# Kernel optimization log

Hardware: AMD Instinct MI355X
Metric: run time of the kernel (lower is better)

The kernel has to match this reference:

```python
import jax, jax.numpy as jnp
import numpy as np

T, H, E, K, I = 4096, 1024, 8, 2, 2048
EPS = 1e-5


def setup_inputs() -> dict:
    key = jax.random.key(0)
    ks = jax.random.split(key, 5)
    xavier = jax.nn.initializers.variance_scaling(1.0, 'fan_avg', 'uniform', dtype=jnp.float32)
    return {
        'x': jax.random.normal(ks[0], (T, H), dtype=jnp.float32),
        'scale': jnp.ones((H,), dtype=jnp.float32),
        'gate_kernel': xavier(ks[1], (H, E), jnp.float32),
        'gate_bias': jnp.zeros((E,), dtype=jnp.float32),
        'mlp1_weight': xavier(ks[2], (E, 2 * I, H), jnp.float32),
        'mlp1_bias': jnp.zeros((E, 2 * I), dtype=jnp.float32),
        'mlp2_weight': xavier(ks[3], (E, H, I), jnp.float32),
        'mlp2_bias': jnp.zeros((E, H), dtype=jnp.float32),
    }


def reference(x, scale, gate_kernel, gate_bias, mlp1_weight, mlp1_bias, mlp2_weight, mlp2_bias):
    # RMSNorm in fp32
    t = x.astype(jnp.float32)
    rms = jnp.sqrt(jnp.mean(t * t, axis=-1, keepdims=True) + EPS)
    normed = ((t / rms) * scale).astype(x.dtype)  # [T, H]

    # Gating: top-k experts + softmax over selected logits
    gate_logits = normed @ gate_kernel + gate_bias  # [T, E]
    expert_logits, expert_indices = jax.lax.top_k(gate_logits, K)  # [T, K]
    expert_weights = jax.nn.softmax(expert_logits, axis=-1)  # [T, K]

    # Dense all-expert SwiGLU MLP (faithful to vmap-over-experts original)
    # mlp1_weight: [E, 2I, H] -> mlp1: [E, T, 2I]
    mlp1 = jnp.einsum('td,efd->etf', normed, mlp1_weight) + mlp1_bias[:, None, :]
    gate_part = jnp.minimum(mlp1[..., :I], 7.0)
    linear_part = jnp.clip(mlp1[..., I:], -7.0, 7.0)
    swish_gate = gate_part * jax.nn.sigmoid(1.702 * gate_part)
    activated = swish_gate * (linear_part + 1.0)  # [E, T, I]
    # mlp2_weight: [E, H, I] -> expert_outputs: [T, E, H]
    expert_outputs = (jnp.einsum('eti,ehi->eth', activated, mlp2_weight)
                      + mlp2_bias[:, None, :]).transpose(1, 0, 2)

    # Scatter top-k weights to dense [T, E] and combine
    one_hot = jax.nn.one_hot(expert_indices, E, dtype=expert_outputs.dtype)  # [T, K, E]
    dense_gate_weights = jnp.sum(one_hot * expert_weights[..., None], axis=1)  # [T, E]
    fused = jnp.einsum('teh,te->th', expert_outputs, dense_gate_weights)
    return x + fused
```

## Files before the change

kernel.cpp:

```cpp
#include <hip/hip_runtime.h>
#include <hip/hip_bf16.h>
#include <math.h>

#define T_ 4096
#define H_ 1024
#define E_ 8
#define I_ 2048
#define EPS_ 1e-5f
#define LDST 72

using bf16x8 = __attribute__((ext_vector_type(8))) short;
using f32x4  = __attribute__((ext_vector_type(4))) float;

static __device__ __forceinline__ unsigned short f2bf(float f) {
    union { float f; unsigned int u; } v; v.f = f;
    unsigned int u = v.u;
    u += 0x7fffu + ((u >> 16) & 1u);
    return (unsigned short)(u >> 16);
}

__global__ __launch_bounds__(256) void k_convert(
    const float* __restrict__ src, unsigned short* __restrict__ dst)
{
    size_t i = (size_t)blockIdx.x * 256 + threadIdx.x;
    const float4* s = (const float4*)src + i * 2;
    float4 a = s[0], b = s[1];
    ushort4 lo, hi;
    lo.x = f2bf(a.x); lo.y = f2bf(a.y); lo.z = f2bf(a.z); lo.w = f2bf(a.w);
    hi.x = f2bf(b.x); hi.y = f2bf(b.y); hi.z = f2bf(b.z); hi.w = f2bf(b.w);
    ((ushort4*)dst)[i * 2]     = lo;
    ((ushort4*)dst)[i * 2 + 1] = hi;
}

__global__ __launch_bounds__(256) void k_norm_gate(
    const float* __restrict__ x, const float* __restrict__ scale,
    const float* __restrict__ gk, const float* __restrict__ gb,
    unsigned short* __restrict__ normed_bf,
    int* __restrict__ counts, int* __restrict__ tok_list, float* __restrict__ w_list)
{
    int tid = threadIdx.x;
    int wave = tid >> 6, lane = tid & 63;
    int t = blockIdx.x * 4 + wave;
    const float* xr = x + (size_t)t * H_;
    int h0 = lane * 16;

    float4 xv[4], sv[4];
    #pragma unroll
    for (int c = 0; c < 4; c++) {
        xv[c] = *(const float4*)(xr + h0 + c * 4);
        sv[c] = *(const float4*)(scale + h0 + c * 4);
    }
    float ss = 0.f;
    #pragma unroll
    for (int c = 0; c < 4; c++)
        ss += xv[c].x*xv[c].x + xv[c].y*xv[c].y + xv[c].z*xv[c].z + xv[c].w*xv[c].w;
    #pragma unroll
    for (int off = 32; off; off >>= 1) ss += __shfl_xor(ss, off);
    float inv = 1.0f / sqrtf(ss / (float)H_ + EPS_);

    float nv[16];
    #pragma unroll
    for (int c = 0; c < 4; c++) {
        nv[c*4+0] = xv[c].x * inv * sv[c].x;
        nv[c*4+1] = xv[c].y * inv * sv[c].y;
        nv[c*4+2] = xv[c].z * inv * sv[c].z;
        nv[c*4+3] = xv[c].w * inv * sv[c].w;
    }
    #pragma unroll
    for (int c = 0; c < 4; c++) {
        ushort4 nb;
        nb.x = f2bf(nv[c*4+0]); nb.y = f2bf(nv[c*4+1]);
        nb.z = f2bf(nv[c*4+2]); nb.w = f2bf(nv[c*4+3]);
        *(ushort4*)(normed_bf + (size_t)t * H_ + h0 + c * 4) = nb;
    }

    float p[E_];
    #pragma unroll
    for (int e = 0; e < E_; e++) p[e] = 0.f;
    #pragma unroll
    for (int j = 0; j < 16; j++) {
        const float4* g4 = (const float4*)(gk + (size_t)(h0 + j) * E_);
        float4 a = g4[0], b = g4[1];
        float n = nv[j];
        p[0] += n*a.x; p[1] += n*a.y; p[2] += n*a.z; p[3] += n*a.w;
        p[4] += n*b.x; p[5] += n*b.y; p[6] += n*b.z; p[7] += n*b.w;
    }
    #pragma unroll
    for (int e = 0; e < E_; e++) {
        #pragma unroll
        for (int off = 32; off; off >>= 1) p[e] += __shfl_xor(p[e], off);
    }
    if (lane == 0) {
        int b0 = -1, b1 = -1; float l0 = -1e30f, l1 = -1e30f;
        #pragma unroll
        for (int e = 0; e < E_; e++) {
            float lg = p[e] + gb[e];
            if (lg > l0) { l1 = l0; b1 = b0; l0 = lg; b0 = e; }
            else if (lg > l1) { l1 = lg; b1 = e; }
        }
        float e1 = expf(l1 - l0);
        float w0 = 1.f / (1.f + e1);
        float w1 = e1 / (1.f + e1);
        int p0 = atomicAdd(&counts[b0], 1);
        tok_list[b0 * T_ + p0] = t * 2 + 0; w_list[b0 * T_ + p0] = w0;
        int p1 = atomicAdd(&counts[b1], 1);
        tok_list[b1 * T_ + p1] = t * 2 + 1; w_list[b1 * T_ + p1] = w1;
    }
}

__global__ __launch_bounds__(256) void k_init_out(
    const float* __restrict__ x, float* __restrict__ out)
{
    size_t i = (size_t)blockIdx.x * 256 + threadIdx.x;
    ((float4*)out)[i] = ((const float4*)x)[i];
}

template<bool PRE>
__global__ __launch_bounds__(256) void k_mlp1(
    const float* __restrict__ w1f, const unsigned short* __restrict__ w1b,
    const float* __restrict__ b1,
    const unsigned short* __restrict__ normed_bf,
    const int* __restrict__ counts, const int* __restrict__ tok_list,
    unsigned short* __restrict__ act)
{
    int e = blockIdx.z;
    int Ne = counts[e];
    int mt0 = blockIdx.y * 64;
    if (mt0 >= Ne) return;
    int it0 = blockIdx.x * 64;
    int tid = threadIdx.x;
    int lane = tid & 63, w = tid >> 6;
    int quad = lane >> 4, m16 = lane & 15;
    int wr = w >> 1, wc = w & 1;

    __shared__ unsigned short lA[64 * LDST];
    __shared__ unsigned short lBg[64 * LDST];
    __shared__ unsigned short lBl[64 * LDST];
    __shared__ int ls_tk[64];

    if (tid < 64) {
        int slot = mt0 + tid;
        ls_tk[tid] = (slot < Ne) ? tok_list[e * T_ + slot] : -1;
    }
    __syncthreads();

    f32x4 accg[2][2], accl[2][2];
    #pragma unroll
    for (int mi = 0; mi < 2; mi++)
        #pragma unroll
        for (int ni = 0; ni < 2; ni++) {
            accg[mi][ni] = (f32x4){0.f, 0.f, 0.f, 0.f};
            accl[mi][ni] = (f32x4){0.f, 0.f, 0.f, 0.f};
        }

    const size_t w1base = (size_t)e * 2 * I_ * H_;
    int rA = tid >> 3, sgA = tid & 7;
    int nB = tid >> 2, sgB = tid & 3;

    if (PRE) {
        int tk0 = ls_tk[rA], tk1 = ls_tk[rA + 32];
        const unsigned short* sA0 = normed_bf + (size_t)((tk0 < 0) ? 0 : (tk0 >> 1)) * H_ + sgA * 8;
        const unsigned short* sA1 = normed_bf + (size_t)((tk1 < 0) ? 0 : (tk1 >> 1)) * H_ + sgA * 8;
        const unsigned short* sG = w1b + w1base + (size_t)(it0 + nB) * H_ + sgB * 16;
        const unsigned short* sL = sG + (size_t)I_ * H_;

        uint4 ra0, ra1, rg0, rg1, rl0, rl1;
        ra0 = (tk0 >= 0) ? *(const uint4*)(sA0) : make_uint4(0,0,0,0);
        ra1 = (tk1 >= 0) ? *(const uint4*)(sA1) : make_uint4(0,0,0,0);
        rg0 = ((const uint4*)sG)[0]; rg1 = ((const uint4*)sG)[1];
        rl0 = ((const uint4*)sL)[0]; rl1 = ((const uint4*)sL)[1];

        for (int kk = 0; kk < H_; kk += 64) {
            __syncthreads();
            *(uint4*)(&lA[rA * LDST + sgA * 8])          = ra0;
            *(uint4*)(&lA[(rA + 32) * LDST + sgA * 8])   = ra1;
            *(uint4*)(&lBg[nB * LDST + sgB * 16])        = rg0;
            *(uint4*)(&lBg[nB * LDST + sgB * 16 + 8])    = rg1;
            *(uint4*)(&lBl[nB * LDST + sgB * 16])        = rl0;
            *(uint4*)(&lBl[nB * LDST + sgB * 16 + 8])    = rl1;
            __syncthreads();
            if (kk + 64 < H_) {
                int k2 = kk + 64;
                ra0 = (tk0 >= 0) ? *(const uint4*)(sA0 + k2) : make_uint4(0,0,0,0);
                ra1 = (tk1 >= 0) ? *(const uint4*)(sA1 + k2) : make_uint4(0,0,0,0);
                rg0 = ((const uint4*)(sG + k2))[0]; rg1 = ((const uint4*)(sG + k2))[1];
                rl0 = ((const uint4*)(sL + k2))[0]; rl1 = ((const uint4*)(sL + k2))[1];
            }
            #pragma unroll
            for (int ks = 0; ks < 64; ks += 32) {
                bf16x8 af[2], bg[2], bl[2];
                #pragma unroll
                for (int mi = 0; mi < 2; mi++)
                    af[mi] = *(const bf16x8*)(&lA[(wr * 32 + mi * 16 + m16) * LDST + ks + quad * 8]);
                #pragma unroll
                for (int ni = 0; ni < 2; ni++) {
                    bg[ni] = *(const bf16x8*)(&lBg[(wc * 32 + ni * 16 + m16) * LDST + ks + quad * 8]);
                    bl[ni] = *(const bf16x8*)(&lBl[(wc * 32 + ni * 16 + m16) * LDST + ks + quad * 8]);
                }
                #pragma unroll
                for (int mi = 0; mi < 2; mi++)
                    #pragma unroll
                    for (int ni = 0; ni < 2; ni++) {
                        accg[mi][ni] = __builtin_amdgcn_mfma_f32_16x16x32_bf16(
                            af[mi], bg[ni], accg[mi][ni], 0, 0, 0);
                        accl[mi][ni] = __builtin_amdgcn_mfma_f32_16x16x32_bf16(
                            af[mi], bl[ni], accl[mi][ni], 0, 0, 0);
                    }
            }
        }
    } else {
        for (int kk = 0; kk < H_; kk += 64) {
            #pragma unroll
            for (int rr = 0; rr < 64; rr += 32) {
                int r = rA + rr;
                int tk = ls_tk[r];
                uint4 v = make_uint4(0u, 0u, 0u, 0u);
                if (tk >= 0)
                    v = *(const uint4*)(normed_bf + (size_t)(tk >> 1) * H_ + kk + sgA * 8);
                *(uint4*)(&lA[r * LDST + sgA * 8]) = v;
            }
            {
                const float* srcg = w1f + w1base + (size_t)(it0 + nB) * H_ + kk + sgB * 16;
                const float* srcl = srcg + (size_t)I_ * H_;
                unsigned short tg[16], tl[16];
                #pragma unroll
                for (int q = 0; q < 4; q++) {
                    float4 fg = ((const float4*)srcg)[q];
                    float4 fl = ((const float4*)srcl)[q];
                    tg[q*4+0] = f2bf(fg.x); tg[q*4+1] = f2bf(fg.y);
                    tg[q*4+2] = f2bf(fg.z); tg[q*4+3] = f2bf(fg.w);
                    tl[q*4+0] = f2bf(fl.x); tl[q*4+1] = f2bf(fl.y);
                    tl[q*4+2] = f2bf(fl.z); tl[q*4+3] = f2bf(fl.w);
                }
                *(uint4*)(&lBg[nB * LDST + sgB * 16])     = *(uint4*)(&tg[0]);
                *(uint4*)(&lBg[nB * LDST + sgB * 16 + 8]) = *(uint4*)(&tg[8]);
                *(uint4*)(&lBl[nB * LDST + sgB * 16])     = *(uint4*)(&tl[0]);
                *(uint4*)(&lBl[nB * LDST + sgB * 16 + 8]) = *(uint4*)(&tl[8]);
            }
            __syncthreads();
            #pragma unroll
            for (int ks = 0; ks < 64; ks += 32) {
                bf16x8 af[2], bg[2], bl[2];
                #pragma unroll
                for (int mi = 0; mi < 2; mi++)
                    af[mi] = *(const bf16x8*)(&lA[(wr * 32 + mi * 16 + m16) * LDST + ks + quad * 8]);
                #pragma unroll
                for (int ni = 0; ni < 2; ni++) {
                    bg[ni] = *(const bf16x8*)(&lBg[(wc * 32 + ni * 16 + m16) * LDST + ks + quad * 8]);
                    bl[ni] = *(const bf16x8*)(&lBl[(wc * 32 + ni * 16 + m16) * LDST + ks + quad * 8]);
                }
                #pragma unroll
                for (int mi = 0; mi < 2; mi++)
                    #pragma unroll
                    for (int ni = 0; ni < 2; ni++) {
                        accg[mi][ni] = __builtin_amdgcn_mfma_f32_16x16x32_bf16(
                            af[mi], bg[ni], accg[mi][ni], 0, 0, 0);
                        accl[mi][ni] = __builtin_amdgcn_mfma_f32_16x16x32_bf16(
                            af[mi], bl[ni], accl[mi][ni], 0, 0, 0);
                    }
            }
            __syncthreads();
        }
    }

    const float* b1g = b1 + (size_t)e * 2 * I_;
    const float* b1l = b1g + I_;
    #pragma unroll
    for (int mi = 0; mi < 2; mi++) {
        #pragma unroll
        for (int reg = 0; reg < 4; reg++) {
            int row = wr * 32 + mi * 16 + quad * 4 + reg;
            int tk = ls_tk[row];
            if (tk < 0) continue;
            #pragma unroll
            for (int ni = 0; ni < 2; ni++) {
                int i = it0 + wc * 32 + ni * 16 + m16;
                float g = accg[mi][ni][reg] + b1g[i];
                float l = accl[mi][ni][reg] + b1l[i];
                g = fminf(g, 7.f);
                l = fminf(fmaxf(l, -7.f), 7.f);
                float sw = g / (1.f + expf(-1.702f * g));
                act[(size_t)tk * I_ + i] = f2bf(sw * (l + 1.f));
            }
        }
    }
}

template<bool PRE>
__global__ __launch_bounds__(256) void k_mlp2(
    const float* __restrict__ w2f, const unsigned short* __restrict__ w2b,
    const float* __restrict__ b2,
    const unsigned short* __restrict__ act,
    const int* __restrict__ counts, const int* __restrict__ tok_list,
    const float* __restrict__ w_list,
    float* __restrict__ out)
{
    int e = blockIdx.z;
    int Ne = counts[e];
    int mt0 = blockIdx.y * 64;
    if (mt0 >= Ne) return;
    int ht0 = blockIdx.x * 128;
    int tid = threadIdx.x;
    int lane = tid & 63, w = tid >> 6;
    int quad = lane >> 4, m16 = lane & 15;
    int wr = w >> 1, wc = w & 1;

    __shared__ unsigned short lA[64 * LDST];
    __shared__ unsigned short lB[128 * LDST];
    __shared__ int ls_tk[64];
    __shared__ float ls_w[64];

    if (tid < 64) {
        int slot = mt0 + tid;
        ls_tk[tid] = (slot < Ne) ? tok_list[e * T_ + slot] : -1;
        ls_w[tid]  = (slot < Ne) ? w_list[e * T_ + slot] : 0.f;
    }
    __syncthreads();

    f32x4 acc[2][4];
    #pragma unroll
    for (int mi = 0; mi < 2; mi++)
        #pragma unroll
        for (int ni = 0; ni < 4; ni++)
            acc[mi][ni] = (f32x4){0.f, 0.f, 0.f, 0.f};

    const size_t w2base = (size_t)e * H_ * I_;
    int rA = tid >> 3, sgA = tid & 7;
    int nB = tid >> 2, sgB = tid & 3;

    if (PRE) {
        int tk0 = ls_tk[rA], tk1 = ls_tk[rA + 32];
        const unsigned short* sA0 = act + (size_t)((tk0 < 0) ? 0 : tk0) * I_ + sgA * 8;
        const unsigned short* sA1 = act + (size_t)((tk1 < 0) ? 0 : tk1) * I_ + sgA * 8;
        const unsigned short* sB0 = w2b + w2base + (size_t)(ht0 + nB) * I_ + sgB * 16;
        const unsigned short* sB1 = sB0 + (size_t)64 * I_;

        uint4 ra0, ra1, rb00, rb01, rb10, rb11;
        ra0 = (tk0 >= 0) ? *(const uint4*)(sA0) : make_uint4(0,0,0,0);
        ra1 = (tk1 >= 0) ? *(const uint4*)(sA1) : make_uint4(0,0,0,0);
        rb00 = ((const uint4*)sB0)[0]; rb01 = ((const uint4*)sB0)[1];
        rb10 = ((const uint4*)sB1)[0]; rb11 = ((const uint4*)sB1)[1];

        for (int kk = 0; kk < I_; kk += 64) {
            __syncthreads();
            *(uint4*)(&lA[rA * LDST + sgA * 8])            = ra0;
            *(uint4*)(&lA[(rA + 32) * LDST + sgA * 8])     = ra1;
            *(uint4*)(&lB[nB * LDST + sgB * 16])           = rb00;
            *(uint4*)(&lB[nB * LDST + sgB * 16 + 8])       = rb01;
            *(uint4*)(&lB[(nB + 64) * LDST + sgB * 16])    = rb10;
            *(uint4*)(&lB[(nB + 64) * LDST + sgB * 16 + 8])= rb11;
            __syncthreads();
            if (kk + 64 < I_) {
                int k2 = kk + 64;
                ra0 = (tk0 >= 0) ? *(const uint4*)(sA0 + k2) : make_uint4(0,0,0,0);
                ra1 = (tk1 >= 0) ? *(const uint4*)(sA1 + k2) : make_uint4(0,0,0,0);
                rb00 = ((const uint4*)(sB0 + k2))[0]; rb01 = ((const uint4*)(sB0 + k2))[1];
                rb10 = ((const uint4*)(sB1 + k2))[0]; rb11 = ((const uint4*)(sB1 + k2))[1];
            }
            #pragma unroll
            for (int ks = 0; ks < 64; ks += 32) {
                bf16x8 af[2], bf[4];
                #pragma unroll
                for (int mi = 0; mi < 2; mi++)
                    af[mi] = *(const bf16x8*)(&lA[(wr * 32 + mi * 16 + m16) * LDST + ks + quad * 8]);
                #pragma unroll
                for (int ni = 0; ni < 4; ni++)
                    bf[ni] = *(const bf16x8*)(&lB[(wc * 64 + ni * 16 + m16) * LDST + ks + quad * 8]);
                #pragma unroll
                for (int mi = 0; mi < 2; mi++)
                    #pragma unroll
                    for (int ni = 0; ni < 4; ni++)
                        acc[mi][ni] = __builtin_amdgcn_mfma_f32_16x16x32_bf16(
                            af[mi], bf[ni], acc[mi][ni], 0, 0, 0);
            }
        }
    } else {
        for (int kk = 0; kk < I_; kk += 64) {
            #pragma unroll
            for (int rr = 0; rr < 64; rr += 32) {
                int r = rA + rr;
                int tk = ls_tk[r];
                uint4 v = make_uint4(0u, 0u, 0u, 0u);
                if (tk >= 0)
                    v = *(const uint4*)(act + (size_t)tk * I_ + kk + sgA * 8);
                *(uint4*)(&lA[r * LDST + sgA * 8]) = v;
            }
            #pragma unroll
            for (int rr = 0; rr < 128; rr += 64) {
                int r = nB + rr;
                const float* src = w2f + w2base + (size_t)(ht0 + r) * I_ + kk + sgB * 16;
                unsigned short tb[16];
                #pragma unroll
                for (int q = 0; q < 4; q++) {
                    float4 f4 = ((const float4*)src)[q];
                    tb[q*4+0] = f2bf(f4.x); tb[q*4+1] = f2bf(f4.y);
                    tb[q*4+2] = f2bf(f4.z); tb[q*4+3] = f2bf(f4.w);
                }
                *(uint4*)(&lB[r * LDST + sgB * 16])     = *(uint4*)(&tb[0]);
                *(uint4*)(&lB[r * LDST + sgB * 16 + 8]) = *(uint4*)(&tb[8]);
            }
            __syncthreads();
            #pragma unroll
            for (int ks = 0; ks < 64; ks += 32) {
                bf16x8 af[2], bf[4];
                #pragma unroll
                for (int mi = 0; mi < 2; mi++)
                    af[mi] = *(const bf16x8*)(&lA[(wr * 32 + mi * 16 + m16) * LDST + ks + quad * 8]);
                #pragma unroll
                for (int ni = 0; ni < 4; ni++)
                    bf[ni] = *(const bf16x8*)(&lB[(wc * 64 + ni * 16 + m16) * LDST + ks + quad * 8]);
                #pragma unroll
                for (int mi = 0; mi < 2; mi++)
                    #pragma unroll
                    for (int ni = 0; ni < 4; ni++)
                        acc[mi][ni] = __builtin_amdgcn_mfma_f32_16x16x32_bf16(
                            af[mi], bf[ni], acc[mi][ni], 0, 0, 0);
            }
            __syncthreads();
        }
    }

    const float* b2e = b2 + (size_t)e * H_;
    #pragma unroll
    for (int mi = 0; mi < 2; mi++) {
        #pragma unroll
        for (int reg = 0; reg < 4; reg++) {
            int row = wr * 32 + mi * 16 + quad * 4 + reg;
            int tk = ls_tk[row];
            if (tk < 0) continue;
            int t = tk >> 1;
            float wgt = ls_w[row];
            #pragma unroll
            for (int ni = 0; ni < 4; ni++) {
                int h = ht0 + wc * 64 + ni * 16 + m16;
                float v = acc[mi][ni][reg] + b2e[h];
                atomicAdd(&out[(size_t)t * H_ + h], wgt * v);
            }
        }
    }
}

extern "C" void kernel_launch(void* const* d_in, const int* in_sizes, int n_in,
                              void* d_out, int out_size, void* d_ws, size_t ws_size,
                              hipStream_t stream) {
    const float* x     = (const float*)d_in[0];
    const float* scale = (const float*)d_in[1];
    const float* gk    = (const float*)d_in[2];
    const float* gb    = (const float*)d_in[3];
    const float* w1    = (const float*)d_in[4];
    const float* b1    = (const float*)d_in[5];
    const float* w2    = (const float*)d_in[6];
    const float* b2    = (const float*)d_in[7];
    float* out = (float*)d_out;

    char* ws = (char*)d_ws;
    const size_t MB = 1024 * 1024;
    bool pre = ws_size >= (size_t)138 * MB;

    unsigned short* normed_bf = (unsigned short*)ws;
    unsigned short* act       = (unsigned short*)(ws + 8 * MB);
    unsigned short* w1b = nullptr;
    unsigned short* w2b = nullptr;
    char* ctl;
    if (pre) {
        w1b = (unsigned short*)(ws + 40 * MB);
        w2b = (unsigned short*)(ws + 104 * MB);
        ctl = ws + 136 * MB;
    } else {
        ctl = ws + 40 * MB;
    }
    int*   counts   = (int*)ctl;
    int*   tok_list = (int*)(ctl + 256);
    float* w_list   = (float*)(ctl + 256 + (size_t)E_ * T_ * 4);

    hipMemsetAsync(counts, 0, E_ * sizeof(int), stream);

    k_norm_gate<<<dim3(T_ / 4), dim3(256), 0, stream>>>(x, scale, gk, gb,
                                                        normed_bf, counts, tok_list, w_list);
    if (pre) {
        k_convert<<<dim3((E_ * 2 * I_ * H_) / (256 * 8)), dim3(256), 0, stream>>>(w1, w1b);
        k_convert<<<dim3((E_ * H_ * I_) / (256 * 8)), dim3(256), 0, stream>>>(w2, w2b);
    }
    k_init_out<<<dim3(T_ * H_ / (256 * 4)), dim3(256), 0, stream>>>(x, out);

    if (pre) {
        k_mlp1<true><<<dim3(I_ / 64, T_ / 64, E_), dim3(256), 0, stream>>>(
            nullptr, w1b, b1, normed_bf, counts, tok_list, act);
        k_mlp2<true><<<dim3(H_ / 128, T_ / 64, E_), dim3(256), 0, stream>>>(
            nullptr, w2b, b2, act, counts, tok_list, w_list, out);
    } else {
        k_mlp1<false><<<dim3(I_ / 64, T_ / 64, E_), dim3(256), 0, stream>>>(
            w1, nullptr, b1, normed_bf, counts, tok_list, act);
        k_mlp2<false><<<dim3(H_ / 128, T_ / 64, E_), dim3(256), 0, stream>>>(
            w2, nullptr, b2, act, counts, tok_list, w_list, out);
    }
}
```

Baseline: 599.8 us.

## Replace atomic scatter with per-slot output buffer and combine; swizzle LDS tiles

The second expert GEMM now writes each token-slot result with its bias to a dense buffer instead of atomically adding weighted results into the output. A new combine kernel then forms x + w0*y0 + w1*y1 per token, and the init-output copy is removed. Shared-memory tiles switch from padded rows to an XOR-swizzled 64-element layout to avoid bank conflicts with less LDS. The fp32-weight fallback path is dropped, so the kernel now assumes a large workspace, and the new buffer reuses memory of the converted first-layer weights.

```diff
diff --git a/kernel.cpp b/kernel.cpp
--- a/kernel.cpp
+++ b/kernel.cpp
@@ -7,7 +7,6 @@
 #define E_ 8
 #define I_ 2048
 #define EPS_ 1e-5f
-#define LDST 72
 
 using bf16x8 = __attribute__((ext_vector_type(8))) short;
 using f32x4  = __attribute__((ext_vector_type(4))) float;
@@ -36,7 +35,7 @@
     const float* __restrict__ x, const float* __restrict__ scale,
     const float* __restrict__ gk, const float* __restrict__ gb,
     unsigned short* __restrict__ normed_bf,
-    int* __restrict__ counts, int* __restrict__ tok_list, float* __restrict__ w_list)
+    int* __restrict__ counts, int* __restrict__ tok_list, float* __restrict__ wtok)
 {
     int tid = threadIdx.x;
     int wave = tid >> 6, lane = tid & 63;
@@ -101,23 +100,17 @@
         float e1 = expf(l1 - l0);
         float w0 = 1.f / (1.f + e1);
         float w1 = e1 / (1.f + e1);
+        wtok[t * 2 + 0] = w0;
+        wtok[t * 2 + 1] = w1;
         int p0 = atomicAdd(&counts[b0], 1);
-        tok_list[b0 * T_ + p0] = t * 2 + 0; w_list[b0 * T_ + p0] = w0;
+        tok_list[b0 * T_ + p0] = t * 2 + 0;
         int p1 = atomicAdd(&counts[b1], 1);
-        tok_list[b1 * T_ + p1] = t * 2 + 1; w_list[b1 * T_ + p1] = w1;
-    }
-}
-
-__global__ __launch_bounds__(256) void k_init_out(
-    const float* __restrict__ x, float* __restrict__ out)
-{
-    size_t i = (size_t)blockIdx.x * 256 + threadIdx.x;
-    ((float4*)out)[i] = ((const float4*)x)[i];
-}
-
-template<bool PRE>
+        tok_list[b1 * T_ + p1] = t * 2 + 1;
+    }
+}
+
 __global__ __launch_bounds__(256) void k_mlp1(
-    const float* __restrict__ w1f, const unsigned short* __restrict__ w1b,
+    const unsigned short* __restrict__ w1b,
     const float* __restrict__ b1,
     const unsigned short* __restrict__ normed_bf,
     const int* __restrict__ counts, const int* __restrict__ tok_list,
@@ -133,9 +126,9 @@
     int quad = lane >> 4, m16 = lane & 15;
     int wr = w >> 1, wc = w & 1;
 
-    __shared__ unsigned short lA[64 * LDST];
-    __shared__ unsigned short lBg[64 * LDST];
-    __shared__ unsigned short lBl[64 * LDST];
+    __shared__ unsigned short lA[64 * 64];
+    __shared__ unsigned short lBg[64 * 64];
+    __shared__ unsigned short lBl[64 * 64];
     __shared__ int ls_tk[64];
 
     if (tid < 64) {
@@ -156,110 +149,60 @@
     const size_t w1base = (size_t)e * 2 * I_ * H_;
     int rA = tid >> 3, sgA = tid & 7;
     int nB = tid >> 2, sgB = tid & 3;
-
-    if (PRE) {
-        int tk0 = ls_tk[rA], tk1 = ls_tk[rA + 32];
-        const unsigned short* sA0 = normed_bf + (size_t)((tk0 < 0) ? 0 : (tk0 >> 1)) * H_ + sgA * 8;
-        const unsigned short* sA1 = normed_bf + (size_t)((tk1 < 0) ? 0 : (tk1 >> 1)) * H_ + sgA * 8;
-        const unsigned short* sG = w1b + w1base + (size_t)(it0 + nB) * H_ + sgB * 16;
-        const unsigned short* sL = sG + (size_t)I_ * H_;
-
-        uint4 ra0, ra1, rg0, rg1, rl0, rl1;
-        ra0 = (tk0 >= 0) ? *(const uint4*)(sA0) : make_uint4(0,0,0,0);
-        ra1 = (tk1 >= 0) ? *(const uint4*)(sA1) : make_uint4(0,0,0,0);
-        rg0 = ((const uint4*)sG)[0]; rg1 = ((const uint4*)sG)[1];
-        rl0 = ((const uint4*)sL)[0]; rl1 = ((const uint4*)sL)[1];
-
-        for (int kk = 0; kk < H_; kk += 64) {
-            __syncthreads();
-            *(uint4*)(&lA[rA * LDST + sgA * 8])          = ra0;
-            *(uint4*)(&lA[(rA + 32) * LDST + sgA * 8])   = ra1;
-            *(uint4*)(&lBg[nB * LDST + sgB * 16])        = rg0;
-            *(uint4*)(&lBg[nB * LDST + sgB * 16 + 8])    = rg1;
-            *(uint4*)(&lBl[nB * LDST + sgB * 16])        = rl0;
-            *(uint4*)(&lBl[nB * LDST + sgB * 16 + 8])    = rl1;
-            __syncthreads();
-            if (kk + 64 < H_) {
-                int k2 = kk + 64;
-                ra0 = (tk0 >= 0) ? *(const uint4*)(sA0 + k2) : make_uint4(0,0,0,0);
-                ra1 = (tk1 >= 0) ? *(const uint4*)(sA1 + k2) : make_uint4(0,0,0,0);
-                rg0 = ((const uint4*)(sG + k2))[0]; rg1 = ((const uint4*)(sG + k2))[1];
-                rl0 = ((const uint4*)(sL + k2))[0]; rl1 = ((const uint4*)(sL + k2))[1];
+    int jA = sgA ^ (rA & 7);
+    int jB0 = (2 * sgB) ^ (nB & 7);
+    int jB1 = (2 * sgB + 1) ^ (nB & 7);
+
+    int tk0 = ls_tk[rA], tk1 = ls_tk[rA + 32];
+    const unsigned short* sA0 = normed_bf + (size_t)((tk0 < 0) ? 0 : (tk0 >> 1)) * H_ + sgA * 8;
+    const unsigned short* sA1 = normed_bf + (size_t)((tk1 < 0) ? 0 : (tk1 >> 1)) * H_ + sgA * 8;
+    const unsigned short* sG = w1b + w1base + (size_t)(it0 + nB) * H_ + sgB * 16;
+    const unsigned short* sL = sG + (size_t)I_ * H_;
+
+    uint4 ra0, ra1, rg0, rg1, rl0, rl1;
+    ra0 = (tk0 >= 0) ? *(const uint4*)(sA0) : make_uint4(0,0,0,0);
+    ra1 = (tk1 >= 0) ? *(const uint4*)(sA1) : make_uint4(0,0,0,0);
+    rg0 = ((const uint4*)sG)[0]; rg1 = ((const uint4*)sG)[1];
+    rl0 = ((const uint4*)sL)[0]; rl1 = ((const uint4*)sL)[1];
+
+    for (int kk = 0; kk < H_; kk += 64) {
+        __syncthreads();
+        *(uint4*)(&lA[rA * 64 + jA * 8])          = ra0;
+        *(uint4*)(&lA[(rA + 32) * 64 + jA * 8])   = ra1;
+        *(uint4*)(&lBg[nB * 64 + jB0 * 8])        = rg0;
+        *(uint4*)(&lBg[nB * 64 + jB1 * 8])        = rg1;
+        *(uint4*)(&lBl[nB * 64 + jB0 * 8])        = rl0;
+        *(uint4*)(&lBl[nB * 64 + jB1 * 8])        = rl1;
+        __syncthreads();
+        if (kk + 64 < H_) {
+            int k2 = kk + 64;
+            ra0 = (tk0 >= 0) ? *(const uint4*)(sA0 + k2) : make_uint4(0,0,0,0);
+            ra1 = (tk1 >= 0) ? *(const uint4*)(sA1 + k2) : make_uint4(0,0,0,0);
+            rg0 = ((const uint4*)(sG + k2))[0]; rg1 = ((const uint4*)(sG + k2))[1];
+            rl0 = ((const uint4*)(sL + k2))[0]; rl1 = ((const uint4*)(sL + k2))[1];
+        }
+        #pragma unroll
+        for (int ks2 = 0; ks2 < 2; ks2++) {
+            int jj = ks2 * 4 + quad;
+            int m7 = m16 & 7;
+            bf16x8 af[2], bg[2], bl[2];
+            #pragma unroll
+            for (int mi = 0; mi < 2; mi++)
+                af[mi] = *(const bf16x8*)(&lA[(wr * 32 + mi * 16 + m16) * 64 + (jj ^ m7) * 8]);
+            #pragma unroll
+            for (int ni = 0; ni < 2; ni++) {
+                bg[ni] = *(const bf16x8*)(&lBg[(wc * 32 + ni * 16 + m16) * 64 + (jj ^ m7) * 8]);
+                bl[ni] = *(const bf16x8*)(&lBl[(wc * 32 + ni * 16 + m16) * 64 + (jj ^ m7) * 8]);
             }
             #pragma unroll
-            for (int ks = 0; ks < 64; ks += 32) {
-                bf16x8 af[2], bg[2], bl[2];
-                #pragma unroll
-                for (int mi = 0; mi < 2; mi++)
-                    af[mi] = *(const bf16x8*)(&lA[(wr * 32 + mi * 16 + m16) * LDST + ks + quad * 8]);
+            for (int mi = 0; mi < 2; mi++)
                 #pragma unroll
                 for (int ni = 0; ni < 2; ni++) {
-                    bg[ni] = *(const bf16x8*)(&lBg[(wc * 32 + ni * 16 + m16) * LDST + ks + quad * 8]);
-                    bl[ni] = *(const bf16x8*)(&lBl[(wc * 32 + ni * 16 + m16) * LDST + ks + quad * 8]);
+                    accg[mi][ni] = __builtin_amdgcn_mfma_f32_16x16x32_bf16(
+                        af[mi], bg[ni], accg[mi][ni], 0, 0, 0);
+                    accl[mi][ni] = __builtin_amdgcn_mfma_f32_16x16x32_bf16(
+                        af[mi], bl[ni], accl[mi][ni], 0, 0, 0);
                 }
-                #pragma unroll
-                for (int mi = 0; mi < 2; mi++)
-                    #pragma unroll
-                    for (int ni = 0; ni < 2; ni++) {
-                        accg[mi][ni] = __builtin_amdgcn_mfma_f32_16x16x32_bf16(
-                            af[mi], bg[ni], accg[mi][ni], 0, 0, 0);
-                        accl[mi][ni] = __builtin_amdgcn_mfma_f32_16x16x32_bf16(
-                            af[mi], bl[ni], accl[mi][ni], 0, 0, 0);
-                    }
-            }
-        }
-    } else {
-        for (int kk = 0; kk < H_; kk += 64) {
-            #pragma unroll
-            for (int rr = 0; rr < 64; rr += 32) {
-                int r = rA + rr;
-                int tk = ls_tk[r];
-                uint4 v = make_uint4(0u, 0u, 0u, 0u);
-                if (tk >= 0)
-                    v = *(const uint4*)(normed_bf + (size_t)(tk >> 1) * H_ + kk + sgA * 8);
-                *(uint4*)(&lA[r * LDST + sgA * 8]) = v;
-            }
-            {
-                const float* srcg = w1f + w1base + (size_t)(it0 + nB) * H_ + kk + sgB * 16;
-                const float* srcl = srcg + (size_t)I_ * H_;
-                unsigned short tg[16], tl[16];
-                #pragma unroll
-                for (int q = 0; q < 4; q++) {
-                    float4 fg = ((const float4*)srcg)[q];
-                    float4 fl = ((const float4*)srcl)[q];
-                    tg[q*4+0] = f2bf(fg.x); tg[q*4+1] = f2bf(fg.y);
-                    tg[q*4+2] = f2bf(fg.z); tg[q*4+3] = f2bf(fg.w);
-                    tl[q*4+0] = f2bf(fl.x); tl[q*4+1] = f2bf(fl.y);
-                    tl[q*4+2] = f2bf(fl.z); tl[q*4+3] = f2bf(fl.w);
-                }
-                *(uint4*)(&lBg[nB * LDST + sgB * 16])     = *(uint4*)(&tg[0]);
-                *(uint4*)(&lBg[nB * LDST + sgB * 16 + 8]) = *(uint4*)(&tg[8]);
-                *(uint4*)(&lBl[nB * LDST + sgB * 16])     = *(uint4*)(&tl[0]);
-                *(uint4*)(&lBl[nB * LDST + sgB * 16 + 8]) = *(uint4*)(&tl[8]);
-            }
-            __syncthreads();
-            #pragma unroll
-            for (int ks = 0; ks < 64; ks += 32) {
-                bf16x8 af[2], bg[2], bl[2];
-                #pragma unroll
-                for (int mi = 0; mi < 2; mi++)
-                    af[mi] = *(const bf16x8*)(&lA[(wr * 32 + mi * 16 + m16) * LDST + ks + quad * 8]);
-                #pragma unroll
-                for (int ni = 0; ni < 2; ni++) {
-                    bg[ni] = *(const bf16x8*)(&lBg[(wc * 32 + ni * 16 + m16) * LDST + ks + quad * 8]);
-                    bl[ni] = *(const bf16x8*)(&lBl[(wc * 32 + ni * 16 + m16) * LDST + ks + quad * 8]);
-                }
-                #pragma unroll
-                for (int mi = 0; mi < 2; mi++)
-                    #pragma unroll
-                    for (int ni = 0; ni < 2; ni++) {
-                        accg[mi][ni] = __builtin_amdgcn_mfma_f32_16x16x32_bf16(
-                            af[mi], bg[ni], accg[mi][ni], 0, 0, 0);
-                        accl[mi][ni] = __builtin_amdgcn_mfma_f32_16x16x32_bf16(
-                            af[mi], bl[ni], accl[mi][ni], 0, 0, 0);
-                    }
-            }
-            __syncthreads();
         }
     }
 
@@ -286,14 +229,12 @@
     }
 }
 
-template<bool PRE>
 __global__ __launch_bounds__(256) void k_mlp2(
-    const float* __restrict__ w2f, const unsigned short* __restrict__ w2b,
+    const unsigned short* __restrict__ w2b,
     const float* __restrict__ b2,
     const unsigned short* __restrict__ act,
     const int* __restrict__ counts, const int* __restrict__ tok_list,
-    const float* __restrict__ w_list,
-    float* __restrict__ out)
+    float* __restrict__ ybuf)
 {
     int e = blockIdx.z;
     int Ne = counts[e];
@@ -305,15 +246,13 @@
     int quad = lane >> 4, m16 = lane & 15;
     int wr = w >> 1, wc = w & 1;
 
-    __shared__ unsigned short lA[64 * LDST];
-    __shared__ unsigned short lB[128 * LDST];
+    __shared__ unsigned short lA[64 * 64];
+    __shared__ unsigned short lB[128 * 64];
     __shared__ int ls_tk[64];
-    __shared__ float ls_w[64];
 
     if (tid < 64) {
         int slot = mt0 + tid;
         ls_tk[tid] = (slot < Ne) ? tok_list[e * T_ + slot] : -1;
-        ls_w[tid]  = (slot < Ne) ? w_list[e * T_ + slot] : 0.f;
     }
     __syncthreads();
 
@@ -327,96 +266,55 @@
     const size_t w2base = (size_t)e * H_ * I_;
     int rA = tid >> 3, sgA = tid & 7;
     int nB = tid >> 2, sgB = tid & 3;
-
-    if (PRE) {
-        int tk0 = ls_tk[rA], tk1 = ls_tk[rA + 32];
-        const unsigned short* sA0 = act + (size_t)((tk0 < 0) ? 0 : tk0) * I_ + sgA * 8;
-        const unsigned short* sA1 = act + (size_t)((tk1 < 0) ? 0 : tk1) * I_ + sgA * 8;
-        const unsigned short* sB0 = w2b + w2base + (size_t)(ht0 + nB) * I_ + sgB * 16;
-        const unsigned short* sB1 = sB0 + (size_t)64 * I_;
-
-        uint4 ra0, ra1, rb00, rb01, rb10, rb11;
-        ra0 = (tk0 >= 0) ? *(const uint4*)(sA0) : make_uint4(0,0,0,0);
-        ra1 = (tk1 >= 0) ? *(const uint4*)(sA1) : make_uint4(0,0,0,0);
-        rb00 = ((const uint4*)sB0)[0]; rb01 = ((const uint4*)sB0)[1];
-        rb10 = ((const uint4*)sB1)[0]; rb11 = ((const uint4*)sB1)[1];
-
-        for (int kk = 0; kk < I_; kk += 64) {
-            __syncthreads();
-            *(uint4*)(&lA[rA * LDST + sgA * 8])            = ra0;
-            *(uint4*)(&lA[(rA + 32) * LDST + sgA * 8])     = ra1;
-            *(uint4*)(&lB[nB * LDST + sgB * 16])           = rb00;
-            *(uint4*)(&lB[nB * LDST + sgB * 16 + 8])       = rb01;
-            *(uint4*)(&lB[(nB + 64) * LDST + sgB * 16])    = rb10;
-            *(uint4*)(&lB[(nB + 64) * LDST + sgB * 16 + 8])= rb11;
-            __syncthreads();
-            if (kk + 64 < I_) {
-                int k2 = kk + 64;
-                ra0 = (tk0 >= 0) ? *(const uint4*)(sA0 + k2) : make_uint4(0,0,0,0);
-                ra1 = (tk1 >= 0) ? *(const uint4*)(sA1 + k2) : make_uint4(0,0,0,0);
-                rb00 = ((const uint4*)(sB0 + k2))[0]; rb01 = ((const uint4*)(sB0 + k2))[1];
-                rb10 = ((const uint4*)(sB1 + k2))[0]; rb11 = ((const uint4*)(sB1 + k2))[1];
-            }
-            #pragma unroll
-            for (int ks = 0; ks < 64; ks += 32) {
-                bf16x8 af[2], bf[4];
-                #pragma unroll
-                for (int mi = 0; mi < 2; mi++)
-                    af[mi] = *(const bf16x8*)(&lA[(wr * 32 + mi * 16 + m16) * LDST + ks + quad * 8]);
+    int jA = sgA ^ (rA & 7);
+    int jB0 = (2 * sgB) ^ (nB & 7);
+    int jB1 = (2 * sgB + 1) ^ (nB & 7);
+
+    int tk0 = ls_tk[rA], tk1 = ls_tk[rA + 32];
+    const unsigned short* sA0 = act + (size_t)((tk0 < 0) ? 0 : tk0) * I_ + sgA * 8;
+    const unsigned short* sA1 = act + (size_t)((tk1 < 0) ? 0 : tk1) * I_ + sgA * 8;
+    const unsigned short* sB0 = w2b + w2base + (size_t)(ht0 + nB) * I_ + sgB * 16;
+    const unsigned short* sB1 = sB0 + (size_t)64 * I_;
+
+    uint4 ra0, ra1, rb00, rb01, rb10, rb11;
+    ra0 = (tk0 >= 0) ? *(const uint4*)(sA0) : make_uint4(0,0,0,0);
+    ra1 = (tk1 >= 0) ? *(const uint4*)(sA1) : make_uint4(0,0,0,0);
+    rb00 = ((const uint4*)sB0)[0]; rb01 = ((const uint4*)sB0)[1];
+    rb10 = ((const uint4*)sB1)[0]; rb11 = ((const uint4*)sB1)[1];
+
+    for (int kk = 0; kk < I_; kk += 64) {
+        __syncthreads();
+        *(uint4*)(&lA[rA * 64 + jA * 8])               = ra0;
+        *(uint4*)(&lA[(rA + 32) * 64 + jA * 8])        = ra1;
+        *(uint4*)(&lB[nB * 64 + jB0 * 8])              = rb00;
+        *(uint4*)(&lB[nB * 64 + jB1 * 8])              = rb01;
+        *(uint4*)(&lB[(nB + 64) * 64 + jB0 * 8])       = rb10;
+        *(uint4*)(&lB[(nB + 64) * 64 + jB1 * 8])       = rb11;
+        __syncthreads();
+        if (kk + 64 < I_) {
+            int k2 = kk + 64;
+            ra0 = (tk0 >= 0) ? *(const uint4*)(sA0 + k2) : make_uint4(0,0,0,0);
+            ra1 = (tk1 >= 0) ? *(const uint4*)(sA1 + k2) : make_uint4(0,0,0,0);
+            rb00 = ((const uint4*)(sB0 + k2))[0]; rb01 = ((const uint4*)(sB0 + k2))[1];
+            rb10 = ((const uint4*)(sB1 + k2))[0]; rb11 = ((const uint4*)(sB1 + k2))[1];
+        }
+        #pragma unroll
+        for (int ks2 = 0; ks2 < 2; ks2++) {
+            int jj = ks2 * 4 + quad;
+            int m7 = m16 & 7;
+            bf16x8 af[2], bf[4];
+            #pragma unroll
+            for (int mi = 0; mi < 2; mi++)
+                af[mi] = *(const bf16x8*)(&lA[(wr * 32 + mi * 16 + m16) * 64 + (jj ^ m7) * 8]);
+            #pragma unroll
+            for (int ni = 0; ni < 4; ni++)
+                bf[ni] = *(const bf16x8*)(&lB[(wc * 64 + ni * 16 + m16) * 64 + (jj ^ m7) * 8]);
+            #pragma unroll
+            for (int mi = 0; mi < 2; mi++)
                 #pragma unroll
                 for (int ni = 0; ni < 4; ni++)
-                    bf[ni] = *(const bf16x8*)(&lB[(wc * 64 + ni * 16 + m16) * LDST + ks + quad * 8]);
-                #pragma unroll
-                for (int mi = 0; mi < 2; mi++)
-                    #pragma unroll
-                    for (int ni = 0; ni < 4; ni++)
-                        acc[mi][ni] = __builtin_amdgcn_mfma_f32_16x16x32_bf16(
-                            af[mi], bf[ni], acc[mi][ni], 0, 0, 0);
-            }
-        }
-    } else {
-        for (int kk = 0; kk < I_; kk += 64) {
-            #pragma unroll
-            for (int rr = 0; rr < 64; rr += 32) {
-                int r = rA + rr;
-                int tk = ls_tk[r];
-                uint4 v = make_uint4(0u, 0u, 0u, 0u);
-                if (tk >= 0)
-                    v = *(const uint4*)(act + (size_t)tk * I_ + kk + sgA * 8);
-                *(uint4*)(&lA[r * LDST + sgA * 8]) = v;
-            }
-            #pragma unroll
-            for (int rr = 0; rr < 128; rr += 64) {
-                int r = nB + rr;
-                const float* src = w2f + w2base + (size_t)(ht0 + r) * I_ + kk + sgB * 16;
-                unsigned short tb[16];
-                #pragma unroll
-                for (int q = 0; q < 4; q++) {
-                    float4 f4 = ((const float4*)src)[q];
-                    tb[q*4+0] = f2bf(f4.x); tb[q*4+1] = f2bf(f4.y);
-                    tb[q*4+2] = f2bf(f4.z); tb[q*4+3] = f2bf(f4.w);
-                }
-                *(uint4*)(&lB[r * LDST + sgB * 16])     = *(uint4*)(&tb[0]);
-                *(uint4*)(&lB[r * LDST + sgB * 16 + 8]) = *(uint4*)(&tb[8]);
-            }
-            __syncthreads();
-            #pragma unroll
-            for (int ks = 0; ks < 64; ks += 32) {
-                bf16x8 af[2], bf[4];
-                #pragma unroll
-                for (int mi = 0; mi < 2; mi++)
-                    af[mi] = *(const bf16x8*)(&lA[(wr * 32 + mi * 16 + m16) * LDST + ks + quad * 8]);
-                #pragma unroll
-                for (int ni = 0; ni < 4; ni++)
-                    bf[ni] = *(const bf16x8*)(&lB[(wc * 64 + ni * 16 + m16) * LDST + ks + quad * 8]);
-                #pragma unroll
-                for (int mi = 0; mi < 2; mi++)
-                    #pragma unroll
-                    for (int ni = 0; ni < 4; ni++)
-                        acc[mi][ni] = __builtin_amdgcn_mfma_f32_16x16x32_bf16(
-                            af[mi], bf[ni], acc[mi][ni], 0, 0, 0);
-            }
-            __syncthreads();
+                    acc[mi][ni] = __builtin_amdgcn_mfma_f32_16x16x32_bf16(
+                        af[mi], bf[ni], acc[mi][ni], 0, 0, 0);
         }
     }
 
@@ -428,16 +326,32 @@
             int row = wr * 32 + mi * 16 + quad * 4 + reg;
             int tk = ls_tk[row];
             if (tk < 0) continue;
-            int t = tk >> 1;
-            float wgt = ls_w[row];
             #pragma unroll
             for (int ni = 0; ni < 4; ni++) {
                 int h = ht0 + wc * 64 + ni * 16 + m16;
-                float v = acc[mi][ni][reg] + b2e[h];
-                atomicAdd(&out[(size_t)t * H_ + h], wgt * v);
+                ybuf[(size_t)tk * H_ + h] = acc[mi][ni][reg] + b2e[h];
             }
         }
     }
+}
+
+__global__ __launch_bounds__(256) void k_combine(
+    const float* __restrict__ x, const float* __restrict__ ybuf,
+    const float* __restrict__ wtok, float* __restrict__ out)
+{
+    int t = blockIdx.x;
+    int tid = threadIdx.x;
+    float w0 = wtok[t * 2 + 0];
+    float w1 = wtok[t * 2 + 1];
+    float4 xv = ((const float4*)(x + (size_t)t * H_))[tid];
+    float4 y0 = ((const float4*)(ybuf + (size_t)(t * 2) * H_))[tid];
+    float4 y1 = ((const float4*)(ybuf + (size_t)(t * 2 + 1) * H_))[tid];
+    float4 o;
+    o.x = xv.x + w0 * y0.x + w1 * y1.x;
+    o.y = xv.y + w0 * y0.y + w1 * y1.y;
+    o.z = xv.z + w0 * y0.z + w1 * y1.z;
+    o.w = xv.w + w0 * y0.w + w1 * y1.w;
+    ((float4*)(out + (size_t)t * H_))[tid] = o;
 }
 
 extern "C" void kernel_launch(void* const* d_in, const int* in_sizes, int n_in,
@@ -455,43 +369,26 @@
 
     char* ws = (char*)d_ws;
     const size_t MB = 1024 * 1024;
-    bool pre = ws_size >= (size_t)138 * MB;
-
     unsigned short* normed_bf = (unsigned short*)ws;
     unsigned short* act       = (unsigned short*)(ws + 8 * MB);
-    unsigned short* w1b = nullptr;
-    unsigned short* w2b = nullptr;
-    char* ctl;
-    if (pre) {
-        w1b = (unsigned short*)(ws + 40 * MB);
-        w2b = (unsigned short*)(ws + 104 * MB);
-        ctl = ws + 136 * MB;
-    } else {
-        ctl = ws + 40 * MB;
-    }
+    unsigned short* w1b       = (unsigned short*)(ws + 40 * MB);
+    float*          ybuf      = (float*)(ws + 40 * MB);
+    unsigned short* w2b       = (unsigned short*)(ws + 104 * MB);
+    char* ctl                 = ws + 136 * MB;
     int*   counts   = (int*)ctl;
     int*   tok_list = (int*)(ctl + 256);
-    float* w_list   = (float*)(ctl + 256 + (size_t)E_ * T_ * 4);
+    float* wtok     = (float*)(ctl + 256 + (size_t)E_ * T_ * 4);
 
     hipMemsetAsync(counts, 0, E_ * sizeof(int), stream);
 
-    k_norm_gate<<<dim3(T_ / 4), dim3(256), 0, stream>>>(x, scale, gk, gb,
-                                                        normed_bf, counts, tok_list, w_list);
-    if (pre) {
-        k_convert<<<dim3((E_ * 2 * I_ * H_) / (256 * 8)), dim3(256), 0, stream>>>(w1, w1b);
-        k_convert<<<dim3((E_ * H_ * I_) / (256 * 8)), dim3(256), 0, stream>>>(w2, w2b);
-    }
-    k_init_out<<<dim3(T_ * H_ / (256 * 4)), dim3(256), 0, stream>>>(x, out);
-
-    if (pre) {
-        k_mlp1<true><<<dim3(I_ / 64, T_ / 64, E_), dim3(256), 0, stream>>>(
-            nullptr, w1b, b1, normed_bf, counts, tok_list, act);
-        k_mlp2<true><<<dim3(H_ / 128, T_ / 64, E_), dim3(256), 0, stream>>>(
-            nullptr, w2b, b2, act, counts, tok_list, w_list, out);
-    } else {
-        k_mlp1<false><<<dim3(I_ / 64, T_ / 64, E_), dim3(256), 0, stream>>>(
-            w1, nullptr, b1, normed_bf, counts, tok_list, act);
-        k_mlp2<false><<<dim3(H_ / 128, T_ / 64, E_), dim3(256), 0, stream>>>(
-            w2, nullptr, b2, act, counts, tok_list, w_list, out);
-    }
-}
+    k_norm_gate<<<dim3(T_ / 4), dim3(256), 0, stream>>>(
+        x, scale, gk, gb, normed_bf, counts, tok_list, wtok);
+    k_convert<<<dim3((E_ * 2 * I_ * H_) / (256 * 8)), dim3(256), 0, stream>>>(w1, w1b);
+    k_convert<<<dim3((E_ * H_ * I_) / (256 * 8)), dim3(256), 0, stream>>>(w2, w2b);
+
+    k_mlp1<<<dim3(I_ / 64, T_ / 64, E_), dim3(256), 0, stream>>>(
+        w1b, b1, normed_bf, counts, tok_list, act);
+    k_mlp2<<<dim3(H_ / 128, T_ / 64, E_), dim3(256), 0, stream>>>(
+        w2b, b2, act, counts, tok_list, ybuf);
+    k_combine<<<dim3(T_), dim3(256), 0, stream>>>(x, ybuf, wtok, out);
+}
```

Result: faster. 567.5 us (-5.4%).
